# Performance work log

Hardware: AMD Instinct MI355X
Metric: run time of the kernel (lower is better)

The kernel has to match this reference:

```python
import jax, jax.numpy as jnp
import numpy as np

N_NODES = 100000
N_EDGES = 1600000
D_IN = 128
D_HID = 128
D_OUT = 1
N_GRAPHS = 64


def setup_inputs() -> dict:
    key = jax.random.key(0)
    ks = jax.random.split(key, 8)
    x = jax.random.normal(ks[0], (N_NODES, D_IN), dtype=jnp.float32)
    edge_index = jax.random.randint(ks[1], (2, N_EDGES), 0, N_NODES, dtype=jnp.int64)
    batch = jnp.sort(jax.random.randint(ks[2], (N_NODES,), 0, N_GRAPHS, dtype=jnp.int64))
    s1 = 1.0 / np.sqrt(D_IN)
    s2 = 1.0 / np.sqrt(D_HID)
    W1 = jax.random.normal(ks[3], (D_IN, D_HID), dtype=jnp.float32) * s1
    b1 = jnp.zeros((D_HID,), dtype=jnp.float32)
    W2 = jax.random.normal(ks[4], (D_HID, D_HID), dtype=jnp.float32) * s2
    b2 = jnp.zeros((D_HID,), dtype=jnp.float32)
    Wf = jax.random.normal(ks[5], (D_HID, D_OUT), dtype=jnp.float32) * s2
    bf = jnp.zeros((D_OUT,), dtype=jnp.float32)
    return {"x": x, "edge_index": edge_index, "batch": batch,
            "W1": W1, "b1": b1, "W2": W2, "b2": b2, "Wf": Wf, "bf": bf,
            "num_graphs": N_GRAPHS}


def reference(x, edge_index, batch, W1, b1, W2, b2, Wf, bf, num_graphs):
    n = x.shape[0]
    # GCNConv default: add self-loops, symmetric deg^{-1/2} normalization
    loop = jnp.arange(n, dtype=edge_index.dtype)
    src = jnp.concatenate([edge_index[0], loop])  # [E+N]
    dst = jnp.concatenate([edge_index[1], loop])
    deg = jax.ops.segment_sum(jnp.ones(src.shape, x.dtype), dst, num_segments=n)
    dinv = jnp.where(deg > 0, jax.lax.rsqrt(jnp.maximum(deg, 1.0)), 0.0)
    norm = dinv[src] * dinv[dst]  # [E+N]

    def gcn_conv(h, W, b):
        h = h @ W  # [N, d_out] linear first (GCNConv fuses lin before propagate)
        msg = h[src] * norm[:, None]  # gather + scale
        return jax.ops.segment_sum(msg, dst, num_segments=n) + b  # scatter-add

    h = jax.nn.relu(gcn_conv(x, W1, b1))
    h = jax.nn.relu(gcn_conv(h, W2, b2))

    # global_mean_pool over batch assignment
    gsum = jax.ops.segment_sum(h, batch, num_segments=num_graphs)
    cnt = jax.ops.segment_sum(jnp.ones((n,), x.dtype), batch, num_segments=num_graphs)
    pooled = gsum / jnp.maximum(cnt, 1.0)[:, None]  # [G, d_hid]

    return (pooled @ Wf + bf).squeeze(-1)  # [G]
```

## Files before the change

### kernel.cpp

```cpp
#include <hip/hip_runtime.h>
#include <hip/hip_bf16.h>
#include <math.h>


#define DFEAT 128
#define SCAN_NB 256
#define SCAN_TPB 256
#define FILL_CHUNKS 256

typedef unsigned int uint32;
typedef __attribute__((ext_vector_type(8))) short bf16x8;
typedef __attribute__((ext_vector_type(4))) float f32x4;

__device__ __forceinline__ uint32 f2bf_rne(float f) {
    uint32 x = __float_as_uint(f);
    return (x + 0x7fffu + ((x >> 16) & 1u)) >> 16;
}
__device__ __forceinline__ uint32 packbf2(float lo, float hi) {
    return f2bf_rne(lo) | (f2bf_rne(hi) << 16);
}
__device__ __forceinline__ float bflo(uint32 u) { return __uint_as_float(u << 16); }
__device__ __forceinline__ float bfhi(uint32 u) { return __uint_as_float(u & 0xffff0000u); }

__global__ void k_zero2(int* __restrict__ a, int* __restrict__ b, int n) {
    int i = blockIdx.x * blockDim.x + threadIdx.x;
    if (i < n) { a[i] = 0; b[i] = 0; }
}

__global__ void k_zero_f(float* __restrict__ p, int n) {
    int i = blockIdx.x * blockDim.x + threadIdx.x;
    if (i < n) p[i] = 0.f;
}

__global__ void k_degcount(const int* __restrict__ dst, int* __restrict__ degcnt, int E) {
    int e = blockIdx.x * blockDim.x + threadIdx.x;
    if (e < E) atomicAdd(&degcnt[dst[e]], 1);
}

__global__ __launch_bounds__(256) void k_wt(const float* __restrict__ W,
                                            unsigned short* __restrict__ Wt) {
    int idx = blockIdx.x * 256 + threadIdx.x;
    if (idx < 128 * 128) {
        int n = idx >> 7, k = idx & 127;
        Wt[idx] = (unsigned short)f2bf_rne(W[(k << 7) + n]);
    }
}

__global__ __launch_bounds__(SCAN_TPB) void k_partsum(const int* __restrict__ deg,
                                                      int* __restrict__ bsum,
                                                      int N, int chunk) {
    int b = blockIdx.x, tid = threadIdx.x;
    int beg = b * chunk, end = min(N, beg + chunk);
    int s = 0;
    for (int i = beg + tid; i < end; i += SCAN_TPB) s += deg[i];
    __shared__ int lds[SCAN_TPB];
    lds[tid] = s;
    __syncthreads();
    for (int off = SCAN_TPB / 2; off > 0; off >>= 1) {
        if (tid < off) lds[tid] += lds[tid + off];
        __syncthreads();
    }
    if (tid == 0) bsum[b] = lds[0];
}

__global__ __launch_bounds__(SCAN_NB) void k_scanb(int* __restrict__ bsum) {
    __shared__ int lds[SCAN_NB];
    int tid = threadIdx.x;
    int v = bsum[tid];
    lds[tid] = v;
    __syncthreads();
    for (int off = 1; off < SCAN_NB; off <<= 1) {
        int t = (tid >= off) ? lds[tid - off] : 0;
        __syncthreads();
        lds[tid] += t;
        __syncthreads();
    }
    bsum[tid] = lds[tid] - v;
}

__global__ __launch_bounds__(SCAN_TPB) void k_writeptr(const int* __restrict__ deg,
                                                       const int* __restrict__ bbase,
                                                       int* __restrict__ rowptr,
                                                       float* __restrict__ dinv,
                                                       int N, int chunk) {
    int b = blockIdx.x, tid = threadIdx.x;
    int beg = b * chunk, end = min(N, beg + chunk);
    int per = (chunk + SCAN_TPB - 1) / SCAN_TPB;
    int tbeg = beg + tid * per;
    int tend = min(end, tbeg + per);
    int s = 0;
    for (int i = tbeg; i < tend; ++i) s += deg[i];
    __shared__ int lds[SCAN_TPB];
    lds[tid] = s;
    __syncthreads();
    for (int off = 1; off < SCAN_TPB; off <<= 1) {
        int t = (tid >= off) ? lds[tid - off] : 0;
        __syncthreads();
        lds[tid] += t;
        __syncthreads();
    }
    int run = bbase[b] + ((tid == 0) ? 0 : lds[tid - 1]);
    for (int i = tbeg; i < tend; ++i) {
        int d = deg[i];
        rowptr[i] = run;
        dinv[i] = rsqrtf((float)(d + 1));
        run += d;
    }
    if (tend == N && tbeg < tend) rowptr[N] = run;
}

__global__ __launch_bounds__(256) void k_fill(const int* __restrict__ src,
                                              const int* __restrict__ dst,
                                              const int* __restrict__ rowptr,
                                              int* __restrict__ fill,
                                              int* __restrict__ col, int E) {
    int r = blockIdx.x & 7;
    int chunk = blockIdx.x >> 3;
    int per = (E + FILL_CHUNKS - 1) / FILL_CHUNKS;
    int beg = chunk * per;
    int end = min(E, beg + per);
    for (int e = beg + threadIdx.x; e < end; e += 256) {
        int d = dst[e];
        if (((d >> 9) & 7) == r) {
            int pos = rowptr[d] + atomicAdd(&fill[d], 1);
            col[pos] = src[e];
        }
    }
}

__global__ __launch_bounds__(256, 3) void k_linear_mfma(const float* __restrict__ H,
                                                        const uint32* __restrict__ Wt,
                                                        uint32* __restrict__ C,
                                                        int N, int ntiles) {
    __shared__ uint32 WtS[128 * 64];
    __shared__ uint32 inS[64 * 64];
    int tid = threadIdx.x;
    int lane = tid & 63;
    int wv = tid >> 6;
    int g = lane >> 4;
    int r = lane & 15;
    int swz = (r & 7) << 4;
    {
        const uint4* srcp = (const uint4*)Wt;
#pragma unroll
        for (int i = 0; i < 8; ++i) {
            int c = tid + i * 256;
            int n = c >> 4, off = c & 15;
            int b = (n * 256 + off * 16) ^ ((n & 7) << 4);
            *(uint4*)((char*)WtS + b) = srcp[c];
        }
    }
    for (int t = blockIdx.x; t < ntiles; t += gridDim.x) {
        int rbase = t << 6;
        __syncthreads();
        {
            const float4* H4 = (const float4*)(H + (size_t)rbase * DFEAT);
            int limrow = N - rbase;
#pragma unroll
            for (int i = 0; i < 4; ++i) {
                int c = tid + i * 256;
                int m = c >> 4, off = c & 15;
                uint4 w2 = make_uint4(0u, 0u, 0u, 0u);
                if (m < limrow) {
                    float4 f0 = H4[m * 32 + off * 2];
                    float4 f1 = H4[m * 32 + off * 2 + 1];
                    w2.x = packbf2(f0.x, f0.y); w2.y = packbf2(f0.z, f0.w);
                    w2.z = packbf2(f1.x, f1.y); w2.w = packbf2(f1.z, f1.w);
                }
                int b = (m * 256 + off * 16) ^ ((m & 7) << 4);
                *(uint4*)((char*)inS + b) = w2;
            }
        }
        __syncthreads();
        f32x4 acc[8];
#pragma unroll
        for (int nt = 0; nt < 8; ++nt) acc[nt] = (f32x4){0.f, 0.f, 0.f, 0.f};
        int mrow = wv * 16 + r;
        const char* inB = (const char*)inS + mrow * 256;
#pragma unroll
        for (int kk = 0; kk < 4; ++kk) {
            int koff = (kk * 64 + g * 16) ^ swz;
            bf16x8 bfrag = *(const bf16x8*)(inB + koff);
#pragma unroll
            for (int nt = 0; nt < 8; ++nt) {
                bf16x8 afrag = *(const bf16x8*)((const char*)WtS + (nt * 16 + r) * 256 + koff);
                acc[nt] = __builtin_amdgcn_mfma_f32_16x16x32_bf16(afrag, bfrag, acc[nt], 0, 0, 0);
            }
        }
        int m = rbase + mrow;
        if (m < N) {
            uint2* Crow = (uint2*)(C + (size_t)m * 64);
#pragma unroll
            for (int nt = 0; nt < 8; ++nt) {
                uint2 u;
                u.x = packbf2(acc[nt].x, acc[nt].y);
                u.y = packbf2(acc[nt].z, acc[nt].w);
                Crow[nt * 4 + g] = u;
            }
        }
    }
}

__global__ __launch_bounds__(256, 3) void k_linear_mfma_b16(const uint4* __restrict__ Hb,
                                                            const uint32* __restrict__ Wt,
                                                            uint32* __restrict__ C,
                                                            int N, int ntiles) {
    __shared__ uint32 WtS[128 * 64];
    __shared__ uint32 inS[64 * 64];
    int tid = threadIdx.x;
    int lane = tid & 63;
    int wv = tid >> 6;
    int g = lane >> 4;
    int r = lane & 15;
    int swz = (r & 7) << 4;
    {
        const uint4* srcp = (const uint4*)Wt;
#pragma unroll
        for (int i = 0; i < 8; ++i) {
            int c = tid + i * 256;
            int n = c >> 4, off = c & 15;
            int b = (n * 256 + off * 16) ^ ((n & 7) << 4);
            *(uint4*)((char*)WtS + b) = srcp[c];
        }
    }
    for (int t = blockIdx.x; t < ntiles; t += gridDim.x) {
        int rbase = t << 6;
        __syncthreads();
        {
            int limrow = N - rbase;
#pragma unroll
            for (int i = 0; i < 4; ++i) {
                int c = tid + i * 256;
                int m = c >> 4, off = c & 15;
                uint4 v = make_uint4(0u, 0u, 0u, 0u);
                if (m < limrow) v = Hb[(size_t)(rbase + m) * 16 + off];
                int b = (m * 256 + off * 16) ^ ((m & 7) << 4);
                *(uint4*)((char*)inS + b) = v;
            }
        }
        __syncthreads();
        f32x4 acc[8];
#pragma unroll
        for (int nt = 0; nt < 8; ++nt) acc[nt] = (f32x4){0.f, 0.f, 0.f, 0.f};
        int mrow = wv * 16 + r;
        const char* inB = (const char*)inS + mrow * 256;
#pragma unroll
        for (int kk = 0; kk < 4; ++kk) {
            int koff = (kk * 64 + g * 16) ^ swz;
            bf16x8 bfrag = *(const bf16x8*)(inB + koff);
#pragma unroll
            for (int nt = 0; nt < 8; ++nt) {
                bf16x8 afrag = *(const bf16x8*)((const char*)WtS + (nt * 16 + r) * 256 + koff);
                acc[nt] = __builtin_amdgcn_mfma_f32_16x16x32_bf16(afrag, bfrag, acc[nt], 0, 0, 0);
            }
        }
        int m = rbase + mrow;
        if (m < N) {
            uint2* Crow = (uint2*)(C + (size_t)m * 64);
#pragma unroll
            for (int nt = 0; nt < 8; ++nt) {
                uint2 u;
                u.x = packbf2(acc[nt].x, acc[nt].y);
                u.y = packbf2(acc[nt].z, acc[nt].w);
                Crow[nt * 4 + g] = u;
            }
        }
    }
}

__global__ __launch_bounds__(256) void k_agg(const uint32* __restrict__ Tb,
                                             uint32* __restrict__ Bout,
                                             const int* __restrict__ col,
                                             const int* __restrict__ rowptr,
                                             const float* __restrict__ dinv,
                                             const float* __restrict__ bias, int N) {
    int lane = threadIdx.x & 63;
    int node = blockIdx.x * 4 + (threadIdx.x >> 6);
    if (node >= N) return;
    float2 b = ((const float2*)bias)[lane];
    float di = dinv[node];
    uint32 us = Tb[(size_t)node * 64 + lane];
    float ws = di * di;
    float2 acc;
    acc.x = bflo(us) * ws;
    acc.y = bfhi(us) * ws;
    int beg = rowptr[node], end = rowptr[node + 1];
    int j = beg;
    for (; j + 3 < end; j += 4) {
        int s0 = col[j + 0];
        int s1 = col[j + 1];
        int s2 = col[j + 2];
        int s3 = col[j + 3];
        float w0 = dinv[s0] * di;
        float w1 = dinv[s1] * di;
        float w2 = dinv[s2] * di;
        float w3 = dinv[s3] * di;
        uint32 u0 = Tb[(size_t)s0 * 64 + lane];
        uint32 u1 = Tb[(size_t)s1 * 64 + lane];
        uint32 u2 = Tb[(size_t)s2 * 64 + lane];
        uint32 u3 = Tb[(size_t)s3 * 64 + lane];
        acc.x += w0 * bflo(u0); acc.y += w0 * bfhi(u0);
        acc.x += w1 * bflo(u1); acc.y += w1 * bfhi(u1);
        acc.x += w2 * bflo(u2); acc.y += w2 * bfhi(u2);
        acc.x += w3 * bflo(u3); acc.y += w3 * bfhi(u3);
    }
    for (; j < end; ++j) {
        int s = col[j];
        float w = dinv[s] * di;
        uint32 u = Tb[(size_t)s * 64 + lane];
        acc.x += w * bflo(u);
        acc.y += w * bfhi(u);
    }
    float ox = fmaxf(acc.x + b.x, 0.f);
    float oy = fmaxf(acc.y + b.y, 0.f);
    Bout[(size_t)node * 64 + lane] = packbf2(ox, oy);
}

__global__ __launch_bounds__(256) void k_pool_sum(const uint32* __restrict__ Hn,
                                                  const int* __restrict__ batch,
                                                  float* __restrict__ gsum,
                                                  int N, int waves_total) {
    int w = blockIdx.x * 4 + (threadIdx.x >> 6);
    int lane = threadIdx.x & 63;
    int per = (N + waves_total - 1) / waves_total;
    int n0 = w * per;
    int n1 = min(N, n0 + per);
    if (n0 >= n1) return;
    int gcur = batch[n0];
    float2 acc = make_float2(0.f, 0.f);
    for (int i = n0; i < n1; ++i) {
        int g = batch[i];
        if (g != gcur) {
            atomicAdd(&gsum[gcur * DFEAT + lane * 2 + 0], acc.x);
            atomicAdd(&gsum[gcur * DFEAT + lane * 2 + 1], acc.y);
            acc = make_float2(0.f, 0.f);
            gcur = g;
        }
        uint32 v = Hn[(size_t)i * 64 + lane];
        acc.x += bflo(v);
        acc.y += bfhi(v);
    }
    atomicAdd(&gsum[gcur * DFEAT + lane * 2 + 0], acc.x);
    atomicAdd(&gsum[gcur * DFEAT + lane * 2 + 1], acc.y);
}

__global__ __launch_bounds__(128) void k_head(const float* __restrict__ gsum,
                                              const int* __restrict__ batch,
                                              const float* __restrict__ Wf,
                                              const float* __restrict__ bf,
                                              float* __restrict__ out, int N) {
    int g = blockIdx.x;
    int tid = threadIdx.x;
    int l = 0, h = N;
    while (l < h) { int m = (l + h) >> 1; if (batch[m] < g) l = m + 1; else h = m; }
    int lo = l;
    h = N;
    while (l < h) { int m = (l + h) >> 1; if (batch[m] < g + 1) l = m + 1; else h = m; }
    int hi = l;
    float cnt = (float)((hi - lo) > 0 ? (hi - lo) : 1);
    float val = (gsum[g * DFEAT + tid] / cnt) * Wf[tid];
    for (int off = 32; off >= 1; off >>= 1) val += __shfl_down(val, off, 64);
    __shared__ float ws2[2];
    if ((tid & 63) == 0) ws2[tid >> 6] = val;
    __syncthreads();
    if (tid == 0) out[g] = ws2[0] + ws2[1] + bf[0];
}

extern "C" void kernel_launch(void* const* d_in, const int* in_sizes, int n_in,
                              void* d_out, int out_size, void* d_ws, size_t ws_size,
                              hipStream_t stream) {
    const float* x    = (const float*)d_in[0];
    const int*   ei   = (const int*)d_in[1];
    const int*   batch= (const int*)d_in[2];
    const float* W1   = (const float*)d_in[3];
    const float* b1   = (const float*)d_in[4];
    const float* W2   = (const float*)d_in[5];
    const float* b2   = (const float*)d_in[6];
    const float* Wf   = (const float*)d_in[7];
    const float* bf   = (const float*)d_in[8];

    int N = in_sizes[0] / DFEAT;
    int E = in_sizes[1] / 2;
    int G = out_size;

    const int* src = ei;
    const int* dst = ei + E;

    char* wsb = (char*)d_ws;
    size_t off = 0;
    auto walloc = [&](size_t bytes) {
        void* p = wsb + off;
        off = (off + bytes + 255) & ~(size_t)255;
        return p;
    };
    uint32* A     = (uint32*)walloc((size_t)N * 64 * sizeof(uint32));
    uint32* B     = (uint32*)walloc((size_t)N * 64 * sizeof(uint32));
    float* dinv   = (float*)walloc((size_t)N * sizeof(float));
    int*   rowptr = (int*)  walloc((size_t)(N + 1) * sizeof(int));
    int*   col    = (int*)  walloc((size_t)E * sizeof(int));
    int*   degcnt = (int*)  walloc((size_t)N * sizeof(int));
    int*   fill   = (int*)  walloc((size_t)N * sizeof(int));
    float* gsum   = (float*)walloc((size_t)G * DFEAT * sizeof(float));
    int*   bsum   = (int*)  walloc((size_t)SCAN_NB * sizeof(int));
    unsigned short* Wt1 = (unsigned short*)walloc(128 * 128 * sizeof(unsigned short));
    unsigned short* Wt2 = (unsigned short*)walloc(128 * 128 * sizeof(unsigned short));
    (void)ws_size; (void)n_in;

    int gN = (N + 255) / 256;
    int gE = (E + 255) / 256;
    int chunk = (N + SCAN_NB - 1) / SCAN_NB;
    int ntiles = (N + 63) >> 6;

    k_zero2<<<gN, 256, 0, stream>>>(degcnt, fill, N);
    k_zero_f<<<(G * DFEAT + 255) / 256, 256, 0, stream>>>(gsum, G * DFEAT);
    k_wt<<<64, 256, 0, stream>>>(W1, Wt1);
    k_wt<<<64, 256, 0, stream>>>(W2, Wt2);
    k_degcount<<<gE, 256, 0, stream>>>(dst, degcnt, E);
    k_partsum<<<SCAN_NB, SCAN_TPB, 0, stream>>>(degcnt, bsum, N, chunk);
    k_scanb<<<1, SCAN_NB, 0, stream>>>(bsum);
    k_writeptr<<<SCAN_NB, SCAN_TPB, 0, stream>>>(degcnt, bsum, rowptr, dinv, N, chunk);
    k_fill<<<FILL_CHUNKS * 8, 256, 0, stream>>>(src, dst, rowptr, fill, col, E);

    k_linear_mfma<<<768, 256, 0, stream>>>(x, (const uint32*)Wt1, A, N, ntiles);
    k_agg<<<(N + 3) / 4, 256, 0, stream>>>(A, B, col, rowptr, dinv, b1, N);
    k_linear_mfma_b16<<<768, 256, 0, stream>>>((const uint4*)B, (const uint32*)Wt2, A, N, ntiles);
    k_agg<<<(N + 3) / 4, 256, 0, stream>>>(A, B, col, rowptr, dinv, b2, N);

    const int POOL_BLOCKS = 1024;
    k_pool_sum<<<POOL_BLOCKS, 256, 0, stream>>>(B, batch, gsum, N, POOL_BLOCKS * 4);
    k_head<<<G, 128, 0, stream>>>(gsum, batch, Wf, bf, (float*)d_out, N);
}
```

Measured before the change: 360.7 us.

## Split transformed features into 8 column slices for cache-local gather

```diff
diff --git a/kernel.cpp b/kernel.cpp
--- a/kernel.cpp
+++ b/kernel.cpp
@@ -131,7 +131,7 @@
 __global__ __launch_bounds__(256, 3) void k_linear_mfma(const float* __restrict__ H,
                                                         const uint32* __restrict__ Wt,
                                                         uint32* __restrict__ C,
-                                                        int N, int ntiles) {
+                                                        int N, int ntiles, size_t sstride) {
     __shared__ uint32 WtS[128 * 64];
     __shared__ uint32 inS[64 * 64];
     int tid = threadIdx.x;
@@ -189,13 +189,12 @@
         }
         int m = rbase + mrow;
         if (m < N) {
-            uint2* Crow = (uint2*)(C + (size_t)m * 64);
 #pragma unroll
             for (int nt = 0; nt < 8; ++nt) {
                 uint2 u;
                 u.x = packbf2(acc[nt].x, acc[nt].y);
                 u.y = packbf2(acc[nt].z, acc[nt].w);
-                Crow[nt * 4 + g] = u;
+                ((uint2*)(C + (size_t)nt * sstride))[(size_t)m * 4 + g] = u;
             }
         }
     }
@@ -204,7 +203,7 @@
 __global__ __launch_bounds__(256, 3) void k_linear_mfma_b16(const uint4* __restrict__ Hb,
                                                             const uint32* __restrict__ Wt,
                                                             uint32* __restrict__ C,
-                                                            int N, int ntiles) {
+                                                            int N, int ntiles, size_t sstride) {
     __shared__ uint32 WtS[128 * 64];
     __shared__ uint32 inS[64 * 64];
     int tid = threadIdx.x;
@@ -256,13 +255,12 @@
         }
         int m = rbase + mrow;
         if (m < N) {
-            uint2* Crow = (uint2*)(C + (size_t)m * 64);
 #pragma unroll
             for (int nt = 0; nt < 8; ++nt) {
                 uint2 u;
                 u.x = packbf2(acc[nt].x, acc[nt].y);
                 u.y = packbf2(acc[nt].z, acc[nt].w);
-                Crow[nt * 4 + g] = u;
+                ((uint2*)(C + (size_t)nt * sstride))[(size_t)m * 4 + g] = u;
             }
         }
     }
@@ -273,13 +271,20 @@
                                              const int* __restrict__ col,
                                              const int* __restrict__ rowptr,
                                              const float* __restrict__ dinv,
-                                             const float* __restrict__ bias, int N) {
+                                             const float* __restrict__ bias,
+                                             int N, size_t sstride) {
+    int slice = blockIdx.x & 7;
+    int nb = blockIdx.x >> 3;
     int lane = threadIdx.x & 63;
-    int node = blockIdx.x * 4 + (threadIdx.x >> 6);
+    int wv = threadIdx.x >> 6;
+    int sub = lane >> 3;
+    int f = lane & 7;
+    int node = (nb * 4 + wv) * 8 + sub;
     if (node >= N) return;
-    float2 b = ((const float2*)bias)[lane];
+    const uint32* T = Tb + (size_t)slice * sstride;
     float di = dinv[node];
-    uint32 us = Tb[(size_t)node * 64 + lane];
+    float2 b = ((const float2*)bias)[slice * 8 + f];
+    uint32 us = T[(size_t)node * 8 + f];
     float ws = di * di;
     float2 acc;
     acc.x = bflo(us) * ws;
@@ -295,10 +300,10 @@
         float w1 = dinv[s1] * di;
         float w2 = dinv[s2] * di;
         float w3 = dinv[s3] * di;
-        uint32 u0 = Tb[(size_t)s0 * 64 + lane];
-        uint32 u1 = Tb[(size_t)s1 * 64 + lane];
-        uint32 u2 = Tb[(size_t)s2 * 64 + lane];
-        uint32 u3 = Tb[(size_t)s3 * 64 + lane];
+        uint32 u0 = T[(size_t)s0 * 8 + f];
+        uint32 u1 = T[(size_t)s1 * 8 + f];
+        uint32 u2 = T[(size_t)s2 * 8 + f];
+        uint32 u3 = T[(size_t)s3 * 8 + f];
         acc.x += w0 * bflo(u0); acc.y += w0 * bfhi(u0);
         acc.x += w1 * bflo(u1); acc.y += w1 * bfhi(u1);
         acc.x += w2 * bflo(u2); acc.y += w2 * bfhi(u2);
@@ -307,13 +312,13 @@
     for (; j < end; ++j) {
         int s = col[j];
         float w = dinv[s] * di;
-        uint32 u = Tb[(size_t)s * 64 + lane];
+        uint32 u = T[(size_t)s * 8 + f];
         acc.x += w * bflo(u);
         acc.y += w * bfhi(u);
     }
     float ox = fmaxf(acc.x + b.x, 0.f);
     float oy = fmaxf(acc.y + b.y, 0.f);
-    Bout[(size_t)node * 64 + lane] = packbf2(ox, oy);
+    Bout[(size_t)node * 64 + slice * 8 + f] = packbf2(ox, oy);
 }
 
 __global__ __launch_bounds__(256) void k_pool_sum(const uint32* __restrict__ Hn,
@@ -393,6 +398,7 @@
         off = (off + bytes + 255) & ~(size_t)255;
         return p;
     };
+    size_t sstride = (size_t)N * 8;
     uint32* A     = (uint32*)walloc((size_t)N * 64 * sizeof(uint32));
     uint32* B     = (uint32*)walloc((size_t)N * 64 * sizeof(uint32));
     float* dinv   = (float*)walloc((size_t)N * sizeof(float));
@@ -410,6 +416,7 @@
     int gE = (E + 255) / 256;
     int chunk = (N + SCAN_NB - 1) / SCAN_NB;
     int ntiles = (N + 63) >> 6;
+    int aggblk = ((N + 31) / 32) * 8;
 
     k_zero2<<<gN, 256, 0, stream>>>(degcnt, fill, N);
     k_zero_f<<<(G * DFEAT + 255) / 256, 256, 0, stream>>>(gsum, G * DFEAT);
@@ -421,10 +428,10 @@
     k_writeptr<<<SCAN_NB, SCAN_TPB, 0, stream>>>(degcnt, bsum, rowptr, dinv, N, chunk);
     k_fill<<<FILL_CHUNKS * 8, 256, 0, stream>>>(src, dst, rowptr, fill, col, E);
 
-    k_linear_mfma<<<768, 256, 0, stream>>>(x, (const uint32*)Wt1, A, N, ntiles);
-    k_agg<<<(N + 3) / 4, 256, 0, stream>>>(A, B, col, rowptr, dinv, b1, N);
-    k_linear_mfma_b16<<<768, 256, 0, stream>>>((const uint4*)B, (const uint32*)Wt2, A, N, ntiles);
-    k_agg<<<(N + 3) / 4, 256, 0, stream>>>(A, B, col, rowptr, dinv, b2, N);
+    k_linear_mfma<<<768, 256, 0, stream>>>(x, (const uint32*)Wt1, A, N, ntiles, sstride);
+    k_agg<<<aggblk, 256, 0, stream>>>(A, B, col, rowptr, dinv, b1, N, sstride);
+    k_linear_mfma_b16<<<768, 256, 0, stream>>>((const uint4*)B, (const uint32*)Wt2, A, N, ntiles, sstride);
+    k_agg<<<aggblk, 256, 0, stream>>>(A, B, col, rowptr, dinv, b2, N, sstride);
 
     const int POOL_BLOCKS = 1024;
     k_pool_sum<<<POOL_BLOCKS, 256, 0, stream>>>(B, batch, gsum, N, POOL_BLOCKS * 4);
```

After: 494.0 us. 1.37x slower.
